# Performance work log

Hardware: AMD Instinct MI355X
Metric: run time of the kernel (lower is better)

The kernel has to match this reference:

```python
import jax, jax.numpy as jnp
import numpy as np

NUM_UNITS = 64
NUM_HEADS = 12
MODEL_UNITS = NUM_UNITS * NUM_HEADS  # 768, must equal input feature dim for residual
EPS = 1e-7  # K.epsilon()


def setup_inputs() -> dict:
    key = jax.random.key(0)
    ks = jax.random.split(key, 7)
    B, T, D = 8, 1024, MODEL_UNITS
    x = jax.random.normal(ks[0], (B, T, D), dtype=jnp.float32)
    mask = jnp.ones((B, T), dtype=bool)
    w_q = jax.random.normal(ks[1], (D, MODEL_UNITS), dtype=jnp.float32) * (D ** -0.5)
    w_k = jax.random.normal(ks[2], (D, MODEL_UNITS), dtype=jnp.float32) * (D ** -0.5)
    w_v = jax.random.normal(ks[3], (D, MODEL_UNITS), dtype=jnp.float32) * (D ** -0.5)
    w_final = jax.random.normal(ks[4], (MODEL_UNITS, MODEL_UNITS), dtype=jnp.float32) * (MODEL_UNITS ** -0.5)
    gamma = jnp.ones((MODEL_UNITS,), dtype=jnp.float32)
    beta = jnp.zeros((MODEL_UNITS,), dtype=jnp.float32)
    return {"x": x, "mask": mask, "w_q": w_q, "w_k": w_k, "w_v": w_v,
            "w_final": w_final, "gamma": gamma, "beta": beta}


def reference(x, mask, w_q, w_k, w_v, w_final, gamma, beta):
    B, T, D = x.shape
    H, U = NUM_HEADS, NUM_UNITS
    # Project and split into heads. Keras split(axis=2) -> head h takes cols h*U:(h+1)*U,
    # which is exactly a reshape [B,T,H,U].
    q = (x @ w_q).reshape(B, T, H, U)
    k = (x @ w_k).reshape(B, T, H, U)
    v = (x @ w_v).reshape(B, T, H, U)
    scale = D ** (-0.5)
    # scores: [B,H,T,T]
    scores = jnp.einsum('bthu,bshu->bhts', q, k) * scale
    m = mask.astype(x.dtype)  # [B,T]
    scores = scores * m[:, None, None, :]  # mask keys
    scores = scores * m[:, None, :, None]  # mask queries
    # sum-normalization (NOT softmax), per source
    scores = scores / (jnp.sum(scores, axis=-1, keepdims=True) + EPS)
    out = jnp.einsum('bhts,bshu->bthu', scores, v).reshape(B, T, H * U)
    out = out @ w_final
    out = out + x  # residual
    # faithful reproduction of source 'normalization' (std is assigned mean — source bug)
    mean = jnp.mean(out, axis=-1, keepdims=True)
    std = mean
    out = gamma * (out - mean) / (std + EPS) + beta
    return out
```

## Files before the change

kernel.cpp:

```cpp
#include <hip/hip_runtime.h>

#define NB 8
#define NT 1024
#define ND 768
#define NH 12
#define NU 64
#define BT (NB*NT)
#define SCALE32 ((float)0.03608439182435161)
#define EPS32 1e-7f

__device__ __forceinline__ float dot64_np(const float* a, const float* b)
{
    float r[4];
#pragma unroll
    for (int j = 0; j < 4; j++) r[j] = __fmul_rn(a[j], b[j]);
#pragma unroll
    for (int i = 1; i < 16; i++)
#pragma unroll
        for (int j = 0; j < 4; j++)
            r[j] = __fadd_rn(r[j], __fmul_rn(a[i * 4 + j], b[i * 4 + j]));
    return __fadd_rn(__fadd_rn(r[0], r[2]), __fadd_rn(r[1], r[3]));
}

__global__ __launch_bounds__(256) void mask_k(
    const unsigned char* __restrict__ mb, float* __restrict__ mf)
{
    __shared__ int cntOff, cntAll;
    if (threadIdx.x == 0) { cntOff = 0; cntAll = 0; }
    __syncthreads();
    int lo = 0, la = 0;
    for (int i = threadIdx.x; i < BT; i += 256)
        if (mb[i] != 0) { la++; if ((i & 3) != 0) lo++; }
    atomicAdd(&cntOff, lo);
    atomicAdd(&cntAll, la);
    __syncthreads();
    const bool int32mode = (cntOff == 0) && (cntAll != 0);
    if (int32mode) {
        const int* mi = (const int*)mb;
        for (int i = threadIdx.x; i < BT; i += 256)
            mf[i] = (mi[i] != 0) ? 1.f : 0.f;
    } else {
        for (int i = threadIdx.x; i < BT; i += 256)
            mf[i] = (mb[i] != 0) ? 1.f : 0.f;
    }
}

__global__ __launch_bounds__(256) void gemmseq(
    const float* __restrict__ A, const float* __restrict__ W,
    const float* __restrict__ R, float* __restrict__ C)
{
    __shared__ float sA[64][68];
    __shared__ float sB[64][68];

    const int t = threadIdx.x;
    const int mbase = blockIdx.x * 64;
    const int nbase = blockIdx.y * 64;
    const int m0 = (t >> 4) * 4;
    const int n0 = (t & 15) * 4;

    float acc[4][4], accA[4][4];
#pragma unroll
    for (int i = 0; i < 4; i++)
#pragma unroll
        for (int j = 0; j < 4; j++) { acc[i][j] = 0.f; accA[i][j] = 0.f; }

    for (int k0 = 0; k0 < 768; k0 += 64) {
        __syncthreads();
#pragma unroll
        for (int i = 0; i < 4; i++) {
            const int idx = t + i * 256;
            const int mr = idx >> 4;
            const int k4 = (idx & 15) * 4;
            const float4 a4 = *(const float4*)&A[(size_t)(mbase + mr) * 768 + k0 + k4];
            sA[k4 + 0][mr] = a4.x;
            sA[k4 + 1][mr] = a4.y;
            sA[k4 + 2][mr] = a4.z;
            sA[k4 + 3][mr] = a4.w;
            *(float4*)&sB[mr][k4] =
                *(const float4*)&W[(size_t)(k0 + mr) * 768 + nbase + k4];
        }
        __syncthreads();

        for (int kk = 0; kk < 64; kk++) {
            float av[4], bv[4];
            *(float4*)&av[0] = *(const float4*)&sA[kk][m0];
            *(float4*)&bv[0] = *(const float4*)&sB[kk][n0];
#pragma unroll
            for (int i = 0; i < 4; i++)
#pragma unroll
                for (int j = 0; j < 4; j++)
                    acc[i][j] = fmaf(av[i], bv[j], acc[i][j]);
        }

        if (k0 + 64 == 384) {
#pragma unroll
            for (int i = 0; i < 4; i++)
#pragma unroll
                for (int j = 0; j < 4; j++) {
                    accA[i][j] = acc[i][j];
                    acc[i][j] = 0.f;
                }
        }
    }

#pragma unroll
    for (int i = 0; i < 4; i++)
#pragma unroll
        for (int j = 0; j < 4; j++) {
            const size_t idx = (size_t)(mbase + m0 + i) * 768 + nbase + n0 + j;
            float o = __fadd_rn(accA[i][j], acc[i][j]);
            if (R) o = __fadd_rn(o, R[idx]);
            C[idx] = o;
        }
}

__global__ __launch_bounds__(128) void denom_np(
    const float* __restrict__ Q, const float* __restrict__ K,
    const float* __restrict__ MF, float* __restrict__ D)
{
    const int gid = blockIdx.x * 128 + threadIdx.x;
    const int bh = gid >> 10;
    const int row = gid & 1023;
    const int b = bh / NH, h = bh % NH;
    const int bh_u = __builtin_amdgcn_readfirstlane(bh);
    const int b_u = bh_u / NH, h_u = bh_u % NH;

    const float mq = MF[b * NT + row];

    float qr[64];
    const float4* qp = (const float4*)&Q[((size_t)(b * NT + row)) * ND + h * 64];
#pragma unroll
    for (int i = 0; i < 16; i++) *(float4*)&qr[i * 4] = qp[i];

    const float* Kb = &K[((size_t)(b_u * NT)) * ND + h_u * 64];
    const float* MFb = &MF[b_u * NT];

    float Bi[8];
    for (int c = 0; c < 8; c++) {
        float b8[8];
        for (int s = 0; s < 128; s++) {
            const int sg = c * 128 + s;
            const float dt = dot64_np(qr, Kb + (size_t)sg * ND);
            float sc = __fmul_rn(dt, SCALE32);
            sc = __fmul_rn(sc, MFb[sg]);
            sc = __fmul_rn(sc, mq);
            const int j = s & 7;
            if (s < 8) b8[j] = sc;
            else       b8[j] = __fadd_rn(b8[j], sc);
        }
        Bi[c] = __fadd_rn(__fadd_rn(__fadd_rn(b8[0], b8[1]), __fadd_rn(b8[2], b8[3])),
                          __fadd_rn(__fadd_rn(b8[4], b8[5]), __fadd_rn(b8[6], b8[7])));
    }

    D[(size_t)bh * NT + row] = __fadd_rn(
        __fadd_rn(__fadd_rn(Bi[0], Bi[1]), __fadd_rn(Bi[2], Bi[3])),
        __fadd_rn(__fadd_rn(Bi[4], Bi[5]), __fadd_rn(Bi[6], Bi[7])));
}

__global__ __launch_bounds__(128) void attn_np(
    const float* __restrict__ K, const float* __restrict__ V,
    const float* __restrict__ D, const float* __restrict__ MF,
    float* __restrict__ QA)
{
    const int gid = blockIdx.x * 128 + threadIdx.x;
    const int bh = gid >> 10;
    const int row = gid & 1023;
    const int b = bh / NH, h = bh % NH;
    const int bh_u = __builtin_amdgcn_readfirstlane(bh);
    const int b_u = bh_u / NH, h_u = bh_u % NH;

    const float mq = MF[b * NT + row];
    const float De = __fadd_rn(D[(size_t)bh * NT + row], EPS32);

    float qr[64];
    const float4* qp = (const float4*)&QA[((size_t)(b * NT + row)) * ND + h * 64];
#pragma unroll
    for (int i = 0; i < 16; i++) *(float4*)&qr[i * 4] = qp[i];

    float o[64];
#pragma unroll
    for (int j = 0; j < 64; j++) o[j] = 0.f;

    const float* Kb = &K[((size_t)(b_u * NT)) * ND + h_u * 64];
    const float* Vb = &V[((size_t)(b_u * NT)) * ND + h_u * 64];
    const float* MFb = &MF[b_u * NT];

    for (int s = 0; s < NT; s++) {
        const float dt = dot64_np(qr, Kb + (size_t)s * ND);
        float sc = __fmul_rn(dt, SCALE32);
        sc = __fmul_rn(sc, MFb[s]);
        sc = __fmul_rn(sc, mq);
        const float p = __fdiv_rn(sc, De);
        const float* vp = Vb + (size_t)s * ND;
#pragma unroll
        for (int j = 0; j < 64; j++)
            o[j] = __fadd_rn(o[j], __fmul_rn(p, vp[j]));
    }

    float4* op = (float4*)&QA[((size_t)(b * NT + row)) * ND + h * 64];
#pragma unroll
    for (int i = 0; i < 16; i++) op[i] = *(float4*)&o[i * 4];
}

__global__ __launch_bounds__(256) void rownorm_np(
    float* __restrict__ Y, const float* __restrict__ gamma,
    const float* __restrict__ beta)
{
    const int wave = threadIdx.x >> 6, lane = threadIdx.x & 63;
    const int row = blockIdx.x * 4 + wave;
    float* yr = Y + (size_t)row * ND;
    const int c = lane >> 3, j = lane & 7;

    const float* a = yr + c * 96;
    float r = a[j];
#pragma unroll
    for (int i = 1; i < 12; i++) r = __fadd_rn(r, a[i * 8 + j]);

    r = __fadd_rn(r, __shfl_xor(r, 1, 64));
    r = __fadd_rn(r, __shfl_xor(r, 2, 64));
    r = __fadd_rn(r, __shfl_xor(r, 4, 64));
    r = __fadd_rn(r, __shfl_xor(r, 8, 64));
    r = __fadd_rn(r, __shfl_xor(r, 16, 64));
    r = __fadd_rn(r, __shfl_xor(r, 32, 64));

    const float m = __fdiv_rn(r, 768.0f);
    const float mpe = __fadd_rn(m, EPS32);

#pragma unroll
    for (int i = 0; i < 12; i++) {
        const int idx = i * 64 + lane;
        const float v = yr[idx];
        float o = __fsub_rn(v, m);
        o = __fmul_rn(gamma[idx], o);
        o = __fdiv_rn(o, mpe);
        o = __fadd_rn(o, beta[idx]);
        yr[idx] = o;
    }
}

extern "C" void kernel_launch(void* const* d_in, const int* in_sizes, int n_in,
                              void* d_out, int out_size, void* d_ws, size_t ws_size,
                              hipStream_t stream)
{
    (void)in_sizes; (void)n_in; (void)out_size; (void)ws_size;
    const float* x     = (const float*)d_in[0];
    const unsigned char* maskb = (const unsigned char*)d_in[1];
    const float* wq    = (const float*)d_in[2];
    const float* wk    = (const float*)d_in[3];
    const float* wv    = (const float*)d_in[4];
    const float* wf    = (const float*)d_in[5];
    const float* gamma = (const float*)d_in[6];
    const float* beta  = (const float*)d_in[7];

    float* ws = (float*)d_ws;
    float* MF = ws;
    float* D  = MF + BT;
    float* Q  = D + (size_t)96 * NT;
    float* K  = Q + (size_t)BT * ND;
    float* V  = K + (size_t)BT * ND;
    float* Y  = (float*)d_out;

    mask_k<<<1, 256, 0, stream>>>(maskb, MF);
    gemmseq<<<dim3(128, 12), 256, 0, stream>>>(x, wq, nullptr, Q);
    gemmseq<<<dim3(128, 12), 256, 0, stream>>>(x, wk, nullptr, K);
    gemmseq<<<dim3(128, 12), 256, 0, stream>>>(x, wv, nullptr, V);
    denom_np<<<768, 128, 0, stream>>>(Q, K, MF, D);
    attn_np<<<768, 128, 0, stream>>>(K, V, D, MF, Q);
    gemmseq<<<dim3(128, 12), 256, 0, stream>>>(Q, wf, x, Y);
    rownorm_np<<<2048, 256, 0, stream>>>(Y, gamma, beta);
}
```

Measured before the change: 1.915 ms.

## Split denominator over key chunks and vectorize K/V loads in attention

The row-sum denominator kernel is split into 3072 blocks, each summing one 128-key chunk, plus a small combine kernel that adds the eight partials in the same order as before. This raises parallelism well above the old 768 blocks of 128 threads. Both attention kernels now read K and V rows as float4 with unroll 2, and the attention kernel uses 256-thread blocks. The explicit readfirstlane scalarization of the batch/head indices is dropped, and an extra workspace buffer plus one more launch are added.

```diff
diff --git a/kernel.cpp b/kernel.cpp
--- a/kernel.cpp
+++ b/kernel.cpp
@@ -8,19 +8,6 @@
 #define BT (NB*NT)
 #define SCALE32 ((float)0.03608439182435161)
 #define EPS32 1e-7f
-
-__device__ __forceinline__ float dot64_np(const float* a, const float* b)
-{
-    float r[4];
-#pragma unroll
-    for (int j = 0; j < 4; j++) r[j] = __fmul_rn(a[j], b[j]);
-#pragma unroll
-    for (int i = 1; i < 16; i++)
-#pragma unroll
-        for (int j = 0; j < 4; j++)
-            r[j] = __fadd_rn(r[j], __fmul_rn(a[i * 4 + j], b[i * 4 + j]));
-    return __fadd_rn(__fadd_rn(r[0], r[2]), __fadd_rn(r[1], r[3]));
-}
 
 __global__ __launch_bounds__(256) void mask_k(
     const unsigned char* __restrict__ mb, float* __restrict__ mf)
@@ -114,60 +101,78 @@
         }
 }
 
-__global__ __launch_bounds__(128) void denom_np(
+__global__ __launch_bounds__(256) void denom_part(
     const float* __restrict__ Q, const float* __restrict__ K,
-    const float* __restrict__ MF, float* __restrict__ D)
-{
-    const int gid = blockIdx.x * 128 + threadIdx.x;
+    const float* __restrict__ MF, float* __restrict__ BiP)
+{
+    const int blk = blockIdx.x;
+    const int bh = blk >> 5;
+    const int C = (blk & 31) >> 2;
+    const int row = (blk & 3) * 256 + threadIdx.x;
+    const int b = bh / NH, h = bh % NH;
+
+    const float mq = MF[b * NT + row];
+
+    float qr[64];
+    const float4* qp = (const float4*)&Q[((size_t)(b * NT + row)) * ND + h * 64];
+#pragma unroll
+    for (int i = 0; i < 16; i++) *(float4*)&qr[i * 4] = qp[i];
+
+    const float* Kb = &K[((size_t)b * NT) * ND + h * 64];
+    const float* MFb = &MF[b * NT];
+
+    float b8[8];
+#pragma unroll 2
+    for (int i = 0; i < 128; i++) {
+        const int s = C * 128 + i;
+        const float4* kp = (const float4*)(Kb + (size_t)s * ND);
+        float4 k4 = kp[0];
+        float r0 = __fmul_rn(qr[0], k4.x);
+        float r1 = __fmul_rn(qr[1], k4.y);
+        float r2 = __fmul_rn(qr[2], k4.z);
+        float r3 = __fmul_rn(qr[3], k4.w);
+#pragma unroll
+        for (int c = 1; c < 16; c++) {
+            k4 = kp[c];
+            r0 = __fadd_rn(r0, __fmul_rn(qr[c * 4 + 0], k4.x));
+            r1 = __fadd_rn(r1, __fmul_rn(qr[c * 4 + 1], k4.y));
+            r2 = __fadd_rn(r2, __fmul_rn(qr[c * 4 + 2], k4.z));
+            r3 = __fadd_rn(r3, __fmul_rn(qr[c * 4 + 3], k4.w));
+        }
+        const float dt = __fadd_rn(__fadd_rn(r0, r2), __fadd_rn(r1, r3));
+        float sc = __fmul_rn(dt, SCALE32);
+        sc = __fmul_rn(sc, MFb[s]);
+        sc = __fmul_rn(sc, mq);
+        const int j = i & 7;
+        if (i < 8) b8[j] = sc;
+        else       b8[j] = __fadd_rn(b8[j], sc);
+    }
+
+    const float Bi = __fadd_rn(
+        __fadd_rn(__fadd_rn(b8[0], b8[1]), __fadd_rn(b8[2], b8[3])),
+        __fadd_rn(__fadd_rn(b8[4], b8[5]), __fadd_rn(b8[6], b8[7])));
+    BiP[((size_t)bh * NT + row) * 8 + C] = Bi;
+}
+
+__global__ __launch_bounds__(256) void denom_comb(
+    const float* __restrict__ BiP, float* __restrict__ D)
+{
+    const int idx = blockIdx.x * 256 + threadIdx.x;
+    const float* p = BiP + (size_t)idx * 8;
+    D[idx] = __fadd_rn(
+        __fadd_rn(__fadd_rn(p[0], p[1]), __fadd_rn(p[2], p[3])),
+        __fadd_rn(__fadd_rn(p[4], p[5]), __fadd_rn(p[6], p[7])));
+}
+
+__global__ __launch_bounds__(256) void attn_np(
+    const float* __restrict__ K, const float* __restrict__ V,
+    const float* __restrict__ D, const float* __restrict__ MF,
+    float* __restrict__ QA)
+{
+    const int gid = blockIdx.x * 256 + threadIdx.x;
     const int bh = gid >> 10;
     const int row = gid & 1023;
     const int b = bh / NH, h = bh % NH;
-    const int bh_u = __builtin_amdgcn_readfirstlane(bh);
-    const int b_u = bh_u / NH, h_u = bh_u % NH;
-
-    const float mq = MF[b * NT + row];
-
-    float qr[64];
-    const float4* qp = (const float4*)&Q[((size_t)(b * NT + row)) * ND + h * 64];
-#pragma unroll
-    for (int i = 0; i < 16; i++) *(float4*)&qr[i * 4] = qp[i];
-
-    const float* Kb = &K[((size_t)(b_u * NT)) * ND + h_u * 64];
-    const float* MFb = &MF[b_u * NT];
-
-    float Bi[8];
-    for (int c = 0; c < 8; c++) {
-        float b8[8];
-        for (int s = 0; s < 128; s++) {
-            const int sg = c * 128 + s;
-            const float dt = dot64_np(qr, Kb + (size_t)sg * ND);
-            float sc = __fmul_rn(dt, SCALE32);
-            sc = __fmul_rn(sc, MFb[sg]);
-            sc = __fmul_rn(sc, mq);
-            const int j = s & 7;
-            if (s < 8) b8[j] = sc;
-            else       b8[j] = __fadd_rn(b8[j], sc);
-        }
-        Bi[c] = __fadd_rn(__fadd_rn(__fadd_rn(b8[0], b8[1]), __fadd_rn(b8[2], b8[3])),
-                          __fadd_rn(__fadd_rn(b8[4], b8[5]), __fadd_rn(b8[6], b8[7])));
-    }
-
-    D[(size_t)bh * NT + row] = __fadd_rn(
-        __fadd_rn(__fadd_rn(Bi[0], Bi[1]), __fadd_rn(Bi[2], Bi[3])),
-        __fadd_rn(__fadd_rn(Bi[4], Bi[5]), __fadd_rn(Bi[6], Bi[7])));
-}
-
-__global__ __launch_bounds__(128) void attn_np(
-    const float* __restrict__ K, const float* __restrict__ V,
-    const float* __restrict__ D, const float* __restrict__ MF,
-    float* __restrict__ QA)
-{
-    const int gid = blockIdx.x * 128 + threadIdx.x;
-    const int bh = gid >> 10;
-    const int row = gid & 1023;
-    const int b = bh / NH, h = bh % NH;
-    const int bh_u = __builtin_amdgcn_readfirstlane(bh);
-    const int b_u = bh_u / NH, h_u = bh_u % NH;
 
     const float mq = MF[b * NT + row];
     const float De = __fadd_rn(D[(size_t)bh * NT + row], EPS32);
@@ -181,20 +186,40 @@
 #pragma unroll
     for (int j = 0; j < 64; j++) o[j] = 0.f;
 
-    const float* Kb = &K[((size_t)(b_u * NT)) * ND + h_u * 64];
-    const float* Vb = &V[((size_t)(b_u * NT)) * ND + h_u * 64];
-    const float* MFb = &MF[b_u * NT];
-
+    const float* Kb = &K[((size_t)b * NT) * ND + h * 64];
+    const float* Vb = &V[((size_t)b * NT) * ND + h * 64];
+    const float* MFb = &MF[b * NT];
+
+#pragma unroll 2
     for (int s = 0; s < NT; s++) {
-        const float dt = dot64_np(qr, Kb + (size_t)s * ND);
+        const float4* kp = (const float4*)(Kb + (size_t)s * ND);
+        const float4* vp = (const float4*)(Vb + (size_t)s * ND);
+        float4 k4 = kp[0];
+        float r0 = __fmul_rn(qr[0], k4.x);
+        float r1 = __fmul_rn(qr[1], k4.y);
+        float r2 = __fmul_rn(qr[2], k4.z);
+        float r3 = __fmul_rn(qr[3], k4.w);
+#pragma unroll
+        for (int c = 1; c < 16; c++) {
+            k4 = kp[c];
+            r0 = __fadd_rn(r0, __fmul_rn(qr[c * 4 + 0], k4.x));
+            r1 = __fadd_rn(r1, __fmul_rn(qr[c * 4 + 1], k4.y));
+            r2 = __fadd_rn(r2, __fmul_rn(qr[c * 4 + 2], k4.z));
+            r3 = __fadd_rn(r3, __fmul_rn(qr[c * 4 + 3], k4.w));
+        }
+        const float dt = __fadd_rn(__fadd_rn(r0, r2), __fadd_rn(r1, r3));
         float sc = __fmul_rn(dt, SCALE32);
         sc = __fmul_rn(sc, MFb[s]);
         sc = __fmul_rn(sc, mq);
         const float p = __fdiv_rn(sc, De);
-        const float* vp = Vb + (size_t)s * ND;
-#pragma unroll
-        for (int j = 0; j < 64; j++)
-            o[j] = __fadd_rn(o[j], __fmul_rn(p, vp[j]));
+#pragma unroll
+        for (int c = 0; c < 16; c++) {
+            const float4 v4 = vp[c];
+            o[c * 4 + 0] = __fadd_rn(o[c * 4 + 0], __fmul_rn(p, v4.x));
+            o[c * 4 + 1] = __fadd_rn(o[c * 4 + 1], __fmul_rn(p, v4.y));
+            o[c * 4 + 2] = __fadd_rn(o[c * 4 + 2], __fmul_rn(p, v4.z));
+            o[c * 4 + 3] = __fadd_rn(o[c * 4 + 3], __fmul_rn(p, v4.w));
+        }
     }
 
     float4* op = (float4*)&QA[((size_t)(b * NT + row)) * ND + h * 64];
@@ -253,19 +278,21 @@
     const float* beta  = (const float*)d_in[7];
 
     float* ws = (float*)d_ws;
-    float* MF = ws;
-    float* D  = MF + BT;
-    float* Q  = D + (size_t)96 * NT;
-    float* K  = Q + (size_t)BT * ND;
-    float* V  = K + (size_t)BT * ND;
-    float* Y  = (float*)d_out;
+    float* MF  = ws;
+    float* D   = MF + BT;
+    float* BiP = D + (size_t)96 * NT;
+    float* Q   = BiP + (size_t)96 * NT * 8;
+    float* K   = Q + (size_t)BT * ND;
+    float* V   = K + (size_t)BT * ND;
+    float* Y   = (float*)d_out;
 
     mask_k<<<1, 256, 0, stream>>>(maskb, MF);
     gemmseq<<<dim3(128, 12), 256, 0, stream>>>(x, wq, nullptr, Q);
     gemmseq<<<dim3(128, 12), 256, 0, stream>>>(x, wk, nullptr, K);
     gemmseq<<<dim3(128, 12), 256, 0, stream>>>(x, wv, nullptr, V);
-    denom_np<<<768, 128, 0, stream>>>(Q, K, MF, D);
-    attn_np<<<768, 128, 0, stream>>>(K, V, D, MF, Q);
+    denom_part<<<3072, 256, 0, stream>>>(Q, K, MF, BiP);
+    denom_comb<<<384, 256, 0, stream>>>(BiP, D);
+    attn_np<<<384, 256, 0, stream>>>(K, V, D, MF, Q);
     gemmseq<<<dim3(128, 12), 256, 0, stream>>>(Q, wf, x, Y);
     rownorm_np<<<2048, 256, 0, stream>>>(Y, gamma, beta);
 }
```

Measured after the change: 3.003 ms. +56.8%, slower.
